# Kernel optimization log

Hardware: AMD Instinct MI355X
Metric: run time of the kernel (lower is better)

## Reference

```python
import jax, jax.numpy as jnp
import numpy as np

INV_148 = 1.0 / 1.48  # scaling to align grids with flat-top gaussian


def _trilinear_sample(grid, pts):
    # grid: [C, D, H, W]; pts: [N, 3] in (x,y,z)=(W,H,D) normalized coords, align_corners=True,
    # padding_mode='zeros' (out-of-bounds corners contribute 0). Returns [C, N].
    C, D, H, W = grid.shape
    fx = (pts[:, 0] + 1.0) * 0.5 * (W - 1)
    fy = (pts[:, 1] + 1.0) * 0.5 * (H - 1)
    fz = (pts[:, 2] + 1.0) * 0.5 * (D - 1)
    x0 = jnp.floor(fx).astype(jnp.int32)
    y0 = jnp.floor(fy).astype(jnp.int32)
    z0 = jnp.floor(fz).astype(jnp.int32)
    wx, wy, wz = fx - x0, fy - y0, fz - z0
    out = jnp.zeros((C, pts.shape[0]), dtype=grid.dtype)
    for dz in (0, 1):
        for dy in (0, 1):
            for dx in (0, 1):
                xi, yi, zi = x0 + dx, y0 + dy, z0 + dz
                w = (wx if dx else 1.0 - wx) * (wy if dy else 1.0 - wy) * (wz if dz else 1.0 - wz)
                valid = ((xi >= 0) & (xi < W) & (yi >= 0) & (yi < H) & (zi >= 0) & (zi < D))
                v = grid[:, jnp.clip(zi, 0, D - 1), jnp.clip(yi, 0, H - 1), jnp.clip(xi, 0, W - 1)]
                out = out + v * (w * valid)
    return out


def setup_inputs() -> dict:
    key = jax.random.key(0)
    ks = jax.random.split(key, 10)
    G, Fch, Dg, N, NPL, OUT = 32, 2, 64, 524288, 64, 1
    in_dim = G * Fch
    x = jax.random.uniform(ks[0], (N, 3), minval=-1.0, maxval=1.0, dtype=jnp.float32)
    grid_scales = jax.random.uniform(ks[1], (G, 3), minval=1.5, maxval=2.5, dtype=jnp.float32)
    grid_translations = jax.random.uniform(ks[2], (G, 3), minval=-1.0, maxval=1.0, dtype=jnp.float32) * (grid_scales - 1.0)
    feature_grids = jax.random.uniform(ks[3], (G, Fch, Dg, Dg, Dg), minval=-0.001, maxval=0.001, dtype=jnp.float32)
    W0 = jax.random.normal(ks[4], (NPL, in_dim), dtype=jnp.float32) * (1.0 / np.sqrt(in_dim))
    b0 = jnp.zeros((NPL,), dtype=jnp.float32)
    W1 = jax.random.normal(ks[5], (NPL, NPL), dtype=jnp.float32) * (1.0 / np.sqrt(NPL))
    b1 = jnp.zeros((NPL,), dtype=jnp.float32)
    W2 = jax.random.normal(ks[6], (OUT, NPL), dtype=jnp.float32) * (1.0 / np.sqrt(NPL))
    b2 = jnp.zeros((OUT,), dtype=jnp.float32)
    return {"x": x, "grid_scales": grid_scales, "grid_translations": grid_translations,
            "feature_grids": feature_grids, "W0": W0, "b0": b0, "W1": W1, "b1": b1, "W2": W2, "b2": b2}


def reference(x, grid_scales, grid_translations, feature_grids, W0, b0, W1, b1, W2, b2):
    G = feature_grids.shape[0]
    N = x.shape[0]
    # transform(): per-grid affine (diag scale + translation), then * 1/1.48 -> [G, N, 3]
    local = (x[None, :, :] * grid_scales[:, None, :] + grid_translations[:, None, :]) * INV_148
    # forward detaches grid coords before grid_sample
    local = jax.lax.stop_gradient(local)
    feats = jax.vmap(_trilinear_sample)(feature_grids, local)  # [G, F, N]
    h = feats.reshape(G * feats.shape[1], N).T  # [N, G*F]
    h = jax.nn.relu(h @ W0.T + b0)
    h = jax.nn.relu(h @ W1.T + b1)
    return h @ W2.T + b2  # [N, n_outputs]
```

## Files before the change

### kernel.cpp

```cpp
#include <hip/hip_runtime.h>
#include <hip/hip_fp16.h>

#define NG    32
#define DG    64
#define NPL   64
#define CPD   8
#define NCELL 512
#define HPAD  16
#define BS    512
#define NPT   3
#define TV    4096

typedef _Float16 half8 __attribute__((ext_vector_type(8)));
typedef float    floatx4 __attribute__((ext_vector_type(4)));

__global__ void pack_grids_kernel(const float* __restrict__ fg,
                                  uint4* __restrict__ pg, int total4) {
    int idx = blockIdx.x * blockDim.x + threadIdx.x;
    if (idx >= total4) return;
    int g  = idx >> 16;
    int v4 = (idx & 65535) << 2;
    const float* base = fg + ((size_t)g << 19);
    float4 a = *(const float4*)(base + v4);
    float4 b = *(const float4*)(base + (1 << 18) + v4);
    uint4 o;
    __half2 h;
    h = __floats2half2_rn(a.x, b.x); o.x = *(unsigned*)&h;
    h = __floats2half2_rn(a.y, b.y); o.y = *(unsigned*)&h;
    h = __floats2half2_rn(a.z, b.z); o.z = *(unsigned*)&h;
    h = __floats2half2_rn(a.w, b.w); o.w = *(unsigned*)&h;
    pg[idx] = o;
}

__device__ __forceinline__ int morton8(int cx, int cy, int cz) {
    return  (cx & 1)              | ((cy & 1) << 1)        | ((cz & 1) << 2)
         | (((cx >> 1) & 1) << 3) | (((cy >> 1) & 1) << 4) | (((cz >> 1) & 1) << 5)
         | (((cx >> 2) & 1) << 6) | (((cy >> 2) & 1) << 7) | (((cz >> 2) & 1) << 8);
}
__device__ __forceinline__ int cell_of(float px, float py, float pz) {
    int cx = min(max((int)((px + 1.0f) * (0.5f * CPD)), 0), CPD - 1);
    int cy = min(max((int)((py + 1.0f) * (0.5f * CPD)), 0), CPD - 1);
    int cz = min(max((int)((pz + 1.0f) * (0.5f * CPD)), 0), CPD - 1);
    return morton8(cx, cy, cz);
}

__global__ __launch_bounds__(BS)
void hist_kernel(const float* __restrict__ x, int N, int* __restrict__ ghist) {
    __shared__ int lh[NCELL];
    for (int i = threadIdx.x; i < NCELL; i += BS) lh[i] = 0;
    __syncthreads();
    int n = blockIdx.x * BS + threadIdx.x;
    if (n < N) atomicAdd(&lh[cell_of(x[3*n], x[3*n+1], x[3*n+2])], 1);
    __syncthreads();
    for (int i = threadIdx.x; i < NCELL; i += BS) {
        int c = lh[i];
        if (c) atomicAdd(&ghist[i * HPAD], c);
    }
}

__global__ __launch_bounds__(NCELL)
void scan_kernel(const int* __restrict__ ghist, int* __restrict__ gcursor,
                 int* __restrict__ cellstart) {
    __shared__ int buf[NCELL];
    int t = threadIdx.x;
    int v = ghist[t * HPAD];
    buf[t] = v;
    __syncthreads();
    #pragma unroll
    for (int off = 1; off < NCELL; off <<= 1) {
        int u = (t >= off) ? buf[t - off] : 0;
        __syncthreads();
        buf[t] += u;
        __syncthreads();
    }
    int excl = buf[t] - v;
    gcursor[t * HPAD] = excl;
    cellstart[t] = excl;
    if (t == NCELL - 1) cellstart[NCELL] = buf[t];
}

__global__ __launch_bounds__(BS)
void scatter_kernel(const float* __restrict__ x, int N,
                    int* __restrict__ gcursor, float4* __restrict__ sorted,
                    int* __restrict__ nidx) {
    __shared__ int cnt[NCELL];
    __shared__ int base[NCELL];
    int tid = threadIdx.x;
    for (int i = tid; i < NCELL; i += BS) cnt[i] = 0;
    __syncthreads();
    int n = blockIdx.x * BS + tid;
    float px = 0.f, py = 0.f, pz = 0.f;
    int c = 0, r = 0;
    bool act = (n < N);
    if (act) {
        px = x[3*n]; py = x[3*n+1]; pz = x[3*n+2];
        c = cell_of(px, py, pz);
        r = atomicAdd(&cnt[c], 1);
    }
    __syncthreads();
    for (int i = tid; i < NCELL; i += BS) {
        int cc = cnt[i];
        base[i] = cc ? atomicAdd(&gcursor[i * HPAD], cc) : 0;
    }
    __syncthreads();
    if (act) {
        int pos = base[c] + r;
        sorted[pos] = make_float4(px, py, pz, 0.0f);
        nidx[pos]   = n;
    }
}

__device__ __forceinline__ float2 h2_to_f2(unsigned u) {
    __half2 h = *reinterpret_cast<__half2*>(&u);
    return __half22float2(h);
}

__global__ __launch_bounds__(BS)
void gather_kernel(const float4* __restrict__ sorted,
                   const int*   __restrict__ cellstart,
                   const float* __restrict__ scales,
                   const float* __restrict__ trans,
                   const unsigned* __restrict__ pg,
                   int4* __restrict__ featbuf, int N)
{
    __shared__ float    sA[NG * 3];
    __shared__ float    sB[NG * 3];
    __shared__ int      sO[NG * 3];
    __shared__ unsigned tile[2][TV];

    const int tid = threadIdx.x;
    int bid = blockIdx.x;
    int c   = ((bid & 7) << 6) + (bid >> 3);

    int s0 = cellstart[c];
    int e  = cellstart[c + 1];

    int cx = (c & 1)        | (((c >> 3) & 1) << 1) | (((c >> 6) & 1) << 2);
    int cy = ((c >> 1) & 1) | (((c >> 4) & 1) << 1) | (((c >> 7) & 1) << 2);
    int cz = ((c >> 2) & 1) | (((c >> 5) & 1) << 1) | (((c >> 8) & 1) << 2);

    if (tid < NG * 3) {
        const float k = (1.0f / 1.48f) * 31.5f;
        float A  = scales[tid] * k;
        float Bv = trans[tid] * k + 31.5f;
        sA[tid] = A; sB[tid] = Bv;
        int d  = tid % 3;
        int cc = (d == 0) ? cx : ((d == 1) ? cy : cz);
        int o  = (int)floorf(fmaf((float)cc * 0.25f - 1.0f, A, Bv));
        sO[tid] = min(max(o, 0), 48);
    }

    float px[NPT], py[NPT], pz[NPT];
    int   ip[NPT];
    bool  act[NPT];
    #pragma unroll
    for (int p = 0; p < NPT; ++p) {
        int i = s0 + (p << 9) + tid;
        ip[p]  = i;
        act[p] = (i < e);
        if (act[p]) {
            float4 q = sorted[i];
            px[p] = q.x; py[p] = q.y; pz[p] = q.z;
        } else { px[p] = py[p] = pz[p] = 0.f; }
    }
    __syncthreads();

    {
        int ox = sO[0], oy = sO[1], oz = sO[2];
        #pragma unroll
        for (int j = 0; j < 8; ++j) {
            int v = tid + (j << 9);
            tile[0][v] = pg[((oz + (v >> 8)) << 12) + ((oy + ((v >> 4) & 15)) << 6)
                            + ox + (v & 15)];
        }
    }
    __syncthreads();

    unsigned fp[NPT][4];
    unsigned r[8];

    #pragma unroll
    for (int g = 0; g < NG; ++g) {
        const int cur = g & 1;

        if (g < NG - 1) {
            int ox = sO[3*g+3], oy = sO[3*g+4], oz = sO[3*g+5];
            const unsigned* gb = pg + ((size_t)(g + 1) << 18);
            #pragma unroll
            for (int j = 0; j < 8; ++j) {
                int v = tid + (j << 9);
                r[j] = gb[((oz + (v >> 8)) << 12) + ((oy + ((v >> 4) & 15)) << 6)
                          + ox + (v & 15)];
            }
        }

        {
            const unsigned* tl = tile[cur];
            float A0 = sA[3*g+0], A1 = sA[3*g+1], A2 = sA[3*g+2];
            float B0 = sB[3*g+0], B1 = sB[3*g+1], B2 = sB[3*g+2];
            int ox = sO[3*g+0], oy = sO[3*g+1], oz = sO[3*g+2];
            #pragma unroll
            for (int p = 0; p < NPT; ++p) {
                if (!act[p]) { fp[p][g & 3] = 0; continue; }
                float fx = fmaf(px[p], A0, B0);
                float fy = fmaf(py[p], A1, B1);
                float fz = fmaf(pz[p], A2, B2);
                float flx = floorf(fx), fly = floorf(fy), flz = floorf(fz);
                int x0 = (int)flx, y0 = (int)fly, z0 = (int)flz;
                float wx = fx - flx, wy = fy - fly, wz = fz - flz;

                float wxa0 = (x0 >= 0  && x0     < DG) ? (1.0f - wx) : 0.0f;
                float wxa1 = (x0 >= -1 && x0 + 1 < DG) ? wx          : 0.0f;
                float wya0 = (y0 >= 0  && y0     < DG) ? (1.0f - wy) : 0.0f;
                float wya1 = (y0 >= -1 && y0 + 1 < DG) ? wy          : 0.0f;
                float wza0 = (z0 >= 0  && z0     < DG) ? (1.0f - wz) : 0.0f;
                float wza1 = (z0 >= -1 && z0 + 1 < DG) ? wz          : 0.0f;

                int ix0 = min(max(x0     - ox, 0), 15);
                int ix1 = min(max(x0 + 1 - ox, 0), 15);
                int iy0 = (min(max(y0     - oy, 0), 15)) << 4;
                int iy1 = (min(max(y0 + 1 - oy, 0), 15)) << 4;
                int iz0 = (min(max(z0     - oz, 0), 15)) << 8;
                int iz1 = (min(max(z0 + 1 - oz, 0), 15)) << 8;

                float w00 = wya0 * wza0, w10 = wya1 * wza0;
                float w01 = wya0 * wza1, w11 = wya1 * wza1;

                float c0 = 0.0f, c1 = 0.0f;
                float2 v;
                v = h2_to_f2(tl[iz0 + iy0 + ix0]); c0 = fmaf(wxa0*w00, v.x, c0); c1 = fmaf(wxa0*w00, v.y, c1);
                v = h2_to_f2(tl[iz0 + iy0 + ix1]); c0 = fmaf(wxa1*w00, v.x, c0); c1 = fmaf(wxa1*w00, v.y, c1);
                v = h2_to_f2(tl[iz0 + iy1 + ix0]); c0 = fmaf(wxa0*w10, v.x, c0); c1 = fmaf(wxa0*w10, v.y, c1);
                v = h2_to_f2(tl[iz0 + iy1 + ix1]); c0 = fmaf(wxa1*w10, v.x, c0); c1 = fmaf(wxa1*w10, v.y, c1);
                v = h2_to_f2(tl[iz1 + iy0 + ix0]); c0 = fmaf(wxa0*w01, v.x, c0); c1 = fmaf(wxa0*w01, v.y, c1);
                v = h2_to_f2(tl[iz1 + iy0 + ix1]); c0 = fmaf(wxa1*w01, v.x, c0); c1 = fmaf(wxa1*w01, v.y, c1);
                v = h2_to_f2(tl[iz1 + iy1 + ix0]); c0 = fmaf(wxa0*w11, v.x, c0); c1 = fmaf(wxa0*w11, v.y, c1);
                v = h2_to_f2(tl[iz1 + iy1 + ix1]); c0 = fmaf(wxa1*w11, v.x, c0); c1 = fmaf(wxa1*w11, v.y, c1);

                __half2 hv = __floats2half2_rn(c0, c1);
                fp[p][g & 3] = *reinterpret_cast<unsigned*>(&hv);
            }
        }

        if (g < NG - 1) {
            #pragma unroll
            for (int j = 0; j < 8; ++j) tile[cur ^ 1][tid + (j << 9)] = r[j];
        }

        if ((g & 3) == 3) {
            const size_t plane = (size_t)(g >> 2) * (size_t)N;
            #pragma unroll
            for (int p = 0; p < NPT; ++p)
                if (act[p])
                    featbuf[plane + ip[p]] =
                        make_int4((int)fp[p][0], (int)fp[p][1],
                                  (int)fp[p][2], (int)fp[p][3]);
        }

        __syncthreads();
    }
}

#define MBS 256
__global__ __launch_bounds__(MBS)
void mlp_kernel(const int4* __restrict__ featbuf,
                const int* __restrict__ nidx,
                const float* __restrict__ W0, const float* __restrict__ b0,
                const float* __restrict__ W1, const float* __restrict__ b1,
                const float* __restrict__ W2, const float* __restrict__ b2,
                float* __restrict__ out, int N)
{
    __shared__ _Float16 sW0h[NPL * NPL];
    __shared__ _Float16 sW1h[NPL * NPL];
    __shared__ float    sb0f[NPL], sb1f[NPL], sW2f[NPL];
    __shared__ _Float16 sH[4][NPL * NPL];

    int tid = threadIdx.x;
    for (int i = tid; i < NPL * NPL; i += MBS) {
        sW0h[i] = (_Float16)W0[i];
        sW1h[i] = (_Float16)W1[i];
    }
    if (tid < NPL) { sb0f[tid] = b0[tid]; sb1f[tid] = b1[tid]; sW2f[tid] = W2[tid]; }
    __syncthreads();

    const int wave = tid >> 6;
    const int lane = tid & 63;
    const int l15  = lane & 15;
    const int kg   = lane >> 4;
    const long wbase = (long)blockIdx.x * MBS + wave * 64;
    if (wbase >= N) return;

    half8 B0[4][2], B1[4][2];
    float bias0[4], bias1[4], w2v[4];
    #pragma unroll
    for (int nt = 0; nt < 4; ++nt) {
        int ch = nt * 16 + l15;
        #pragma unroll
        for (int kh = 0; kh < 2; ++kh) {
            int k = kh * 32 + kg * 8;
            B0[nt][kh] = *(const half8*)&sW0h[ch * NPL + k];
            B1[nt][kh] = *(const half8*)&sW1h[ch * NPL + k];
        }
        bias0[nt] = sb0f[ch];
        bias1[nt] = sb1f[ch];
        w2v[nt]   = sW2f[ch];
    }

    _Float16* H = &sH[wave][0];

    floatx4 acc[4][4];
    #pragma unroll
    for (int mt = 0; mt < 4; ++mt) {
        long pt = wbase + mt * 16 + l15;
        if (pt > N - 1) pt = N - 1;
        int4 t0 = featbuf[(size_t)kg * N + pt];
        int4 t1 = featbuf[(size_t)(4 + kg) * N + pt];
        half8 a0 = *reinterpret_cast<half8*>(&t0);
        half8 a1 = *reinterpret_cast<half8*>(&t1);
        #pragma unroll
        for (int nt = 0; nt < 4; ++nt) {
            floatx4 cc = {0.f, 0.f, 0.f, 0.f};
            cc = __builtin_amdgcn_mfma_f32_16x16x32_f16(a0, B0[nt][0], cc, 0, 0, 0);
            cc = __builtin_amdgcn_mfma_f32_16x16x32_f16(a1, B0[nt][1], cc, 0, 0, 0);
            acc[mt][nt] = cc;
        }
    }
    #pragma unroll
    for (int mt = 0; mt < 4; ++mt)
        #pragma unroll
        for (int nt = 0; nt < 4; ++nt) {
            int ch = nt * 16 + l15;
            #pragma unroll
            for (int r = 0; r < 4; ++r) {
                float v = fmaxf(acc[mt][nt][r] + bias0[nt], 0.0f);
                H[(mt * 16 + kg * 4 + r) * NPL + ch] = (_Float16)v;
            }
        }

    floatx4 acc2[4][4];
    #pragma unroll
    for (int mt = 0; mt < 4; ++mt) {
        const _Float16* hp = &H[(mt * 16 + l15) * NPL];
        half8 a0 = *(const half8*)&hp[kg * 8];
        half8 a1 = *(const half8*)&hp[32 + kg * 8];
        #pragma unroll
        for (int nt = 0; nt < 4; ++nt) {
            floatx4 cc = {0.f, 0.f, 0.f, 0.f};
            cc = __builtin_amdgcn_mfma_f32_16x16x32_f16(a0, B1[nt][0], cc, 0, 0, 0);
            cc = __builtin_amdgcn_mfma_f32_16x16x32_f16(a1, B1[nt][1], cc, 0, 0, 0);
            acc2[mt][nt] = cc;
        }
    }

    float p[4][4];
    #pragma unroll
    for (int mt = 0; mt < 4; ++mt)
        #pragma unroll
        for (int r = 0; r < 4; ++r) p[mt][r] = 0.0f;
    #pragma unroll
    for (int mt = 0; mt < 4; ++mt)
        #pragma unroll
        for (int nt = 0; nt < 4; ++nt)
            #pragma unroll
            for (int r = 0; r < 4; ++r) {
                float v = fmaxf(acc2[mt][nt][r] + bias1[nt], 0.0f);
                p[mt][r] = fmaf(v, w2v[nt], p[mt][r]);
            }
    #pragma unroll
    for (int mt = 0; mt < 4; ++mt)
        #pragma unroll
        for (int r = 0; r < 4; ++r) {
            float s = p[mt][r];
            s += __shfl_xor(s, 1);
            s += __shfl_xor(s, 2);
            s += __shfl_xor(s, 4);
            s += __shfl_xor(s, 8);
            p[mt][r] = s;
        }

    float* HF = (float*)H;
    float ob = b2[0];
    if (l15 == 0) {
        #pragma unroll
        for (int mt = 0; mt < 4; ++mt)
            #pragma unroll
            for (int r = 0; r < 4; ++r)
                HF[mt * 16 + kg * 4 + r] = p[mt][r] + ob;
    }
    long pos = wbase + lane;
    if (pos < N) out[nidx[pos]] = HF[lane];
}

__global__ __launch_bounds__(256)
void fused_fallback_kernel(const float* __restrict__ x,
                           const float* __restrict__ scales,
                           const float* __restrict__ trans,
                           const __half2* __restrict__ pg,
                           const float* __restrict__ W0, const float* __restrict__ b0,
                           const float* __restrict__ W1, const float* __restrict__ b1,
                           const float* __restrict__ W2, const float* __restrict__ b2,
                           float* __restrict__ out, int N)
{
    __shared__ float sW0[NPL*NPL], sW1[NPL*NPL], sW2[NPL], sb0[NPL], sb1[NPL];
    __shared__ float sA[NG*3], sB[NG*3];
    const int tid = threadIdx.x;
    for (int i = tid; i < NPL*NPL; i += 256) { sW0[i] = W0[i]; sW1[i] = W1[i]; }
    if (tid < NPL) { sW2[tid] = W2[tid]; sb0[tid] = b0[tid]; sb1[tid] = b1[tid]; }
    if (tid < NG*3) {
        const float k = (1.0f / 1.48f) * 31.5f;
        sA[tid] = scales[tid] * k;
        sB[tid] = trans[tid] * k + 31.5f;
    }
    __syncthreads();
    int n = blockIdx.x * 256 + tid;
    if (n >= N) return;
    float px = x[3*n], py = x[3*n+1], pz = x[3*n+2];
    float feat[2*NG];
    #pragma unroll
    for (int g = 0; g < NG; ++g) {
        float fx = fmaf(px, sA[3*g+0], sB[3*g+0]);
        float fy = fmaf(py, sA[3*g+1], sB[3*g+1]);
        float fz = fmaf(pz, sA[3*g+2], sB[3*g+2]);
        float c0 = 0.f, c1 = 0.f;
        if (fx > -1.f && fx < 64.f && fy > -1.f && fy < 64.f && fz > -1.f && fz < 64.f) {
            float flx = floorf(fx), fly = floorf(fy), flz = floorf(fz);
            int x0 = (int)flx, y0 = (int)fly, z0 = (int)flz;
            float wx = fx-flx, wy = fy-fly, wz = fz-flz;
            float wxa[2], wya[2], wza[2]; int xia[2], yia[2], zia[2];
            wxa[0] = (x0 >= 0  && x0   < DG) ? (1.f-wx) : 0.f;
            wxa[1] = (x0 >= -1 && x0+1 < DG) ? wx : 0.f;
            wya[0] = (y0 >= 0  && y0   < DG) ? (1.f-wy) : 0.f;
            wya[1] = (y0 >= -1 && y0+1 < DG) ? wy : 0.f;
            wza[0] = (z0 >= 0  && z0   < DG) ? (1.f-wz) : 0.f;
            wza[1] = (z0 >= -1 && z0+1 < DG) ? wz : 0.f;
            xia[0] = min(max(x0,0),DG-1); xia[1] = min(max(x0+1,0),DG-1);
            yia[0] = min(max(y0,0),DG-1); yia[1] = min(max(y0+1,0),DG-1);
            zia[0] = min(max(z0,0),DG-1); zia[1] = min(max(z0+1,0),DG-1);
            #pragma unroll
            for (int dz = 0; dz < 2; ++dz)
                #pragma unroll
                for (int dy = 0; dy < 2; ++dy) {
                    int rowoff = (zia[dz] << 12) + (yia[dy] << 6);
                    float wyz = wya[dy] * wza[dz];
                    #pragma unroll
                    for (int dx = 0; dx < 2; ++dx) {
                        float w = wxa[dx] * wyz;
                        float2 vf = __half22float2(pg[(g << 18) + rowoff + xia[dx]]);
                        c0 = fmaf(w, vf.x, c0); c1 = fmaf(w, vf.y, c1);
                    }
                }
        }
        feat[2*g] = c0; feat[2*g+1] = c1;
    }
    float h1[NPL];
    #pragma unroll
    for (int j = 0; j < NPL; j += 2) {
        float a0=0.f,a1=0.f,a2=0.f,a3=0.f;
        const float* r0 = &sW0[j*NPL]; const float* r1 = &sW0[(j+1)*NPL];
        #pragma unroll
        for (int k = 0; k < NPL; k += 2) {
            a0 = fmaf(feat[k],r0[k],a0); a1 = fmaf(feat[k+1],r0[k+1],a1);
            a2 = fmaf(feat[k],r1[k],a2); a3 = fmaf(feat[k+1],r1[k+1],a3);
        }
        h1[j] = fmaxf((a0+a1)+sb0[j],0.f); h1[j+1] = fmaxf((a2+a3)+sb0[j+1],0.f);
    }
    #pragma unroll
    for (int j = 0; j < NPL; j += 2) {
        float a0=0.f,a1=0.f,a2=0.f,a3=0.f;
        const float* r0 = &sW1[j*NPL]; const float* r1 = &sW1[(j+1)*NPL];
        #pragma unroll
        for (int k = 0; k < NPL; k += 2) {
            a0 = fmaf(h1[k],r0[k],a0); a1 = fmaf(h1[k+1],r0[k+1],a1);
            a2 = fmaf(h1[k],r1[k],a2); a3 = fmaf(h1[k+1],r1[k+1],a3);
        }
        feat[j] = fmaxf((a0+a1)+sb1[j],0.f); feat[j+1] = fmaxf((a2+a3)+sb1[j+1],0.f);
    }
    float a0 = 0.f, a1 = 0.f;
    #pragma unroll
    for (int k = 0; k < NPL; k += 2) { a0 = fmaf(feat[k],sW2[k],a0); a1 = fmaf(feat[k+1],sW2[k+1],a1); }
    out[n] = (a0+a1) + b2[0];
}

extern "C" void kernel_launch(void* const* d_in, const int* in_sizes, int n_in,
                              void* d_out, int out_size, void* d_ws, size_t ws_size,
                              hipStream_t stream) {
    const float* x  = (const float*)d_in[0];
    const float* gs = (const float*)d_in[1];
    const float* gt = (const float*)d_in[2];
    const float* fg = (const float*)d_in[3];
    const float* W0 = (const float*)d_in[4];
    const float* b0 = (const float*)d_in[5];
    const float* W1 = (const float*)d_in[6];
    const float* b1 = (const float*)d_in[7];
    const float* W2 = (const float*)d_in[8];
    const float* b2 = (const float*)d_in[9];
    float* out = (float*)d_out;

    const int N = out_size;

    const size_t pg_bytes   = (size_t)NG * (1 << 18) * 4;
    const size_t feat_bytes = (size_t)N * 8 * sizeof(int4);
    const size_t sort_bytes = (size_t)N * sizeof(float4);
    const size_t nidx_bytes = (size_t)N * sizeof(int);
    const size_t cs_bytes   = ((NCELL + 1 + 15) & ~15) * sizeof(int);
    const size_t hist_bytes = (size_t)NCELL * HPAD * sizeof(int);
    const size_t need_full  = pg_bytes + feat_bytes + sort_bytes + nidx_bytes
                            + cs_bytes + 2 * hist_bytes;

    if (ws_size >= need_full) {
        char* w = (char*)d_ws;
        unsigned* pg        = (unsigned*)w;  w += pg_bytes;
        int4*     featbuf   = (int4*)w;      w += feat_bytes;
        float4*   sorted    = (float4*)w;    w += sort_bytes;
        int*      nidx      = (int*)w;       w += nidx_bytes;
        int*      cellstart = (int*)w;       w += cs_bytes;
        int*      ghist     = (int*)w;       w += hist_bytes;
        int*      gcur      = (int*)w;

        int total4 = NG << 16;
        int nblk   = (N + BS - 1) / BS;
        pack_grids_kernel<<<(total4 + 255) / 256, 256, 0, stream>>>(fg, (uint4*)pg, total4);
        hipMemsetAsync(ghist, 0, hist_bytes, stream);
        hist_kernel<<<nblk, BS, 0, stream>>>(x, N, ghist);
        scan_kernel<<<1, NCELL, 0, stream>>>(ghist, gcur, cellstart);
        scatter_kernel<<<nblk, BS, 0, stream>>>(x, N, gcur, sorted, nidx);
        gather_kernel<<<NCELL, BS, 0, stream>>>(
            sorted, cellstart, gs, gt, pg, featbuf, N);
        mlp_kernel<<<(N + MBS - 1) / MBS, MBS, 0, stream>>>(
            featbuf, nidx, W0, b0, W1, b1, W2, b2, out, N);
    } else if (ws_size >= pg_bytes) {
        unsigned* pg = (unsigned*)d_ws;
        int total4 = NG << 16;
        pack_grids_kernel<<<(total4 + 255) / 256, 256, 0, stream>>>(fg, (uint4*)pg, total4);
        fused_fallback_kernel<<<(N + 255) / 256, 256, 0, stream>>>(
            x, gs, gt, (const __half2*)pg, W0, b0, W1, b1, W2, b2, out, N);
    } else {
        fused_fallback_kernel<<<(N + 255) / 256, 256, 0, stream>>>(
            x, gs, gt, (const __half2*)fg, W0, b0, W1, b1, W2, b2, out, N);
    }
}
```

Baseline: 185.7 us.

## Sort into finer cells, split gather blocks, skip out-of-range grids per cell

After: 189.3 us. No clear change (+2.0%).

```diff
diff --git a/kernel.cpp b/kernel.cpp
--- a/kernel.cpp
+++ b/kernel.cpp
@@ -4,12 +4,13 @@
 #define NG    32
 #define DG    64
 #define NPL   64
-#define CPD   8
+#define CPD2  16
+#define NC2   4096
 #define NCELL 512
-#define HPAD  16
+#define HPAD  4
 #define BS    512
-#define NPT   3
 #define TV    4096
+#define HS    68
 
 typedef _Float16 half8 __attribute__((ext_vector_type(8)));
 typedef float    floatx4 __attribute__((ext_vector_type(4)));
@@ -32,61 +33,70 @@
     pg[idx] = o;
 }
 
-__device__ __forceinline__ int morton8(int cx, int cy, int cz) {
-    return  (cx & 1)              | ((cy & 1) << 1)        | ((cz & 1) << 2)
-         | (((cx >> 1) & 1) << 3) | (((cy >> 1) & 1) << 4) | (((cz >> 1) & 1) << 5)
-         | (((cx >> 2) & 1) << 6) | (((cy >> 2) & 1) << 7) | (((cz >> 2) & 1) << 8);
+__device__ __forceinline__ int morton16(int cx, int cy, int cz) {
+    int m = 0;
+    #pragma unroll
+    for (int b = 0; b < 4; ++b)
+        m |= (((cx >> b) & 1) << (3 * b))
+           | (((cy >> b) & 1) << (3 * b + 1))
+           | (((cz >> b) & 1) << (3 * b + 2));
+    return m;
 }
 __device__ __forceinline__ int cell_of(float px, float py, float pz) {
-    int cx = min(max((int)((px + 1.0f) * (0.5f * CPD)), 0), CPD - 1);
-    int cy = min(max((int)((py + 1.0f) * (0.5f * CPD)), 0), CPD - 1);
-    int cz = min(max((int)((pz + 1.0f) * (0.5f * CPD)), 0), CPD - 1);
-    return morton8(cx, cy, cz);
+    int cx = min(max((int)((px + 1.0f) * (0.5f * CPD2)), 0), CPD2 - 1);
+    int cy = min(max((int)((py + 1.0f) * (0.5f * CPD2)), 0), CPD2 - 1);
+    int cz = min(max((int)((pz + 1.0f) * (0.5f * CPD2)), 0), CPD2 - 1);
+    return morton16(cx, cy, cz);
 }
 
 __global__ __launch_bounds__(BS)
 void hist_kernel(const float* __restrict__ x, int N, int* __restrict__ ghist) {
-    __shared__ int lh[NCELL];
-    for (int i = threadIdx.x; i < NCELL; i += BS) lh[i] = 0;
+    __shared__ int lh[NC2];
+    for (int i = threadIdx.x; i < NC2; i += BS) lh[i] = 0;
     __syncthreads();
     int n = blockIdx.x * BS + threadIdx.x;
     if (n < N) atomicAdd(&lh[cell_of(x[3*n], x[3*n+1], x[3*n+2])], 1);
     __syncthreads();
-    for (int i = threadIdx.x; i < NCELL; i += BS) {
+    for (int i = threadIdx.x; i < NC2; i += BS) {
         int c = lh[i];
         if (c) atomicAdd(&ghist[i * HPAD], c);
     }
 }
 
-__global__ __launch_bounds__(NCELL)
+__global__ __launch_bounds__(1024)
 void scan_kernel(const int* __restrict__ ghist, int* __restrict__ gcursor,
                  int* __restrict__ cellstart) {
-    __shared__ int buf[NCELL];
+    __shared__ int tsum[1024];
     int t = threadIdx.x;
-    int v = ghist[t * HPAD];
-    buf[t] = v;
-    __syncthreads();
-    #pragma unroll
-    for (int off = 1; off < NCELL; off <<= 1) {
-        int u = (t >= off) ? buf[t - off] : 0;
+    int v0 = ghist[(t * 4 + 0) * HPAD];
+    int v1 = ghist[(t * 4 + 1) * HPAD];
+    int v2 = ghist[(t * 4 + 2) * HPAD];
+    int v3 = ghist[(t * 4 + 3) * HPAD];
+    tsum[t] = v0 + v1 + v2 + v3;
+    __syncthreads();
+    #pragma unroll
+    for (int off = 1; off < 1024; off <<= 1) {
+        int u = (t >= off) ? tsum[t - off] : 0;
         __syncthreads();
-        buf[t] += u;
+        tsum[t] += u;
         __syncthreads();
     }
-    int excl = buf[t] - v;
-    gcursor[t * HPAD] = excl;
-    cellstart[t] = excl;
-    if (t == NCELL - 1) cellstart[NCELL] = buf[t];
+    int base = (t == 0) ? 0 : tsum[t - 1];
+    gcursor[(t*4+0)*HPAD] = base; cellstart[t*4+0] = base; base += v0;
+    gcursor[(t*4+1)*HPAD] = base; cellstart[t*4+1] = base; base += v1;
+    gcursor[(t*4+2)*HPAD] = base; cellstart[t*4+2] = base; base += v2;
+    gcursor[(t*4+3)*HPAD] = base; cellstart[t*4+3] = base;
+    if (t == 1023) cellstart[NC2] = tsum[1023];
 }
 
 __global__ __launch_bounds__(BS)
 void scatter_kernel(const float* __restrict__ x, int N,
                     int* __restrict__ gcursor, float4* __restrict__ sorted,
                     int* __restrict__ nidx) {
-    __shared__ int cnt[NCELL];
-    __shared__ int base[NCELL];
+    __shared__ int cnt[NC2];
+    __shared__ int base[NC2];
     int tid = threadIdx.x;
-    for (int i = tid; i < NCELL; i += BS) cnt[i] = 0;
+    for (int i = tid; i < NC2; i += BS) cnt[i] = 0;
     __syncthreads();
     int n = blockIdx.x * BS + tid;
     float px = 0.f, py = 0.f, pz = 0.f;
@@ -98,7 +108,7 @@
         r = atomicAdd(&cnt[c], 1);
     }
     __syncthreads();
-    for (int i = tid; i < NCELL; i += BS) {
+    for (int i = tid; i < NC2; i += BS) {
         int cc = cnt[i];
         base[i] = cc ? atomicAdd(&gcursor[i * HPAD], cc) : 0;
     }
@@ -115,9 +125,61 @@
     return __half22float2(h);
 }
 
+template<bool FAST>
+__device__ __forceinline__ unsigned sample_tile(
+    const unsigned* __restrict__ tl,
+    float px, float py, float pz,
+    float A0, float A1, float A2, float B0, float B1, float B2,
+    int ox, int oy, int oz)
+{
+    float fx = fmaf(px, A0, B0);
+    float fy = fmaf(py, A1, B1);
+    float fz = fmaf(pz, A2, B2);
+    float flx = floorf(fx), fly = floorf(fy), flz = floorf(fz);
+    int x0 = (int)flx, y0 = (int)fly, z0 = (int)flz;
+    float wx = fx - flx, wy = fy - fly, wz = fz - flz;
+
+    float wxa0, wxa1, wya0, wya1, wza0, wza1;
+    if (FAST) {
+        wxa0 = 1.0f - wx; wxa1 = wx;
+        wya0 = 1.0f - wy; wya1 = wy;
+        wza0 = 1.0f - wz; wza1 = wz;
+    } else {
+        wxa0 = (x0 >= 0  && x0     < DG) ? (1.0f - wx) : 0.0f;
+        wxa1 = (x0 >= -1 && x0 + 1 < DG) ? wx          : 0.0f;
+        wya0 = (y0 >= 0  && y0     < DG) ? (1.0f - wy) : 0.0f;
+        wya1 = (y0 >= -1 && y0 + 1 < DG) ? wy          : 0.0f;
+        wza0 = (z0 >= 0  && z0     < DG) ? (1.0f - wz) : 0.0f;
+        wza1 = (z0 >= -1 && z0 + 1 < DG) ? wz          : 0.0f;
+    }
+    int ix0 = min(max(x0     - ox, 0), 15);
+    int ix1 = min(max(x0 + 1 - ox, 0), 15);
+    int iy0 = (min(max(y0     - oy, 0), 15)) << 4;
+    int iy1 = (min(max(y0 + 1 - oy, 0), 15)) << 4;
+    int iz0 = (min(max(z0     - oz, 0), 15)) << 8;
+    int iz1 = (min(max(z0 + 1 - oz, 0), 15)) << 8;
+
+    float w00 = wya0 * wza0, w10 = wya1 * wza0;
+    float w01 = wya0 * wza1, w11 = wya1 * wza1;
+
+    float c0 = 0.0f, c1 = 0.0f;
+    float2 v;
+    v = h2_to_f2(tl[iz0+iy0+ix0]); c0 = fmaf(wxa0*w00, v.x, c0); c1 = fmaf(wxa0*w00, v.y, c1);
+    v = h2_to_f2(tl[iz0+iy0+ix1]); c0 = fmaf(wxa1*w00, v.x, c0); c1 = fmaf(wxa1*w00, v.y, c1);
+    v = h2_to_f2(tl[iz0+iy1+ix0]); c0 = fmaf(wxa0*w10, v.x, c0); c1 = fmaf(wxa0*w10, v.y, c1);
+    v = h2_to_f2(tl[iz0+iy1+ix1]); c0 = fmaf(wxa1*w10, v.x, c0); c1 = fmaf(wxa1*w10, v.y, c1);
+    v = h2_to_f2(tl[iz1+iy0+ix0]); c0 = fmaf(wxa0*w01, v.x, c0); c1 = fmaf(wxa0*w01, v.y, c1);
+    v = h2_to_f2(tl[iz1+iy0+ix1]); c0 = fmaf(wxa1*w01, v.x, c0); c1 = fmaf(wxa1*w01, v.y, c1);
+    v = h2_to_f2(tl[iz1+iy1+ix0]); c0 = fmaf(wxa0*w11, v.x, c0); c1 = fmaf(wxa0*w11, v.y, c1);
+    v = h2_to_f2(tl[iz1+iy1+ix1]); c0 = fmaf(wxa1*w11, v.x, c0); c1 = fmaf(wxa1*w11, v.y, c1);
+
+    __half2 hv = __floats2half2_rn(c0, c1);
+    return *reinterpret_cast<unsigned*>(&hv);
+}
+
 __global__ __launch_bounds__(BS)
 void gather_kernel(const float4* __restrict__ sorted,
-                   const int*   __restrict__ cellstart,
+                   const int*   __restrict__ cs16,
                    const float* __restrict__ scales,
                    const float* __restrict__ trans,
                    const unsigned* __restrict__ pg,
@@ -126,14 +188,23 @@
     __shared__ float    sA[NG * 3];
     __shared__ float    sB[NG * 3];
     __shared__ int      sO[NG * 3];
+    __shared__ int      sCls[NG];
+    __shared__ int      sList[NG + 1];
     __shared__ unsigned tile[2][TV];
 
-    const int tid = threadIdx.x;
-    int bid = blockIdx.x;
-    int c   = ((bid & 7) << 6) + (bid >> 3);
-
-    int s0 = cellstart[c];
-    int e  = cellstart[c + 1];
+    const int tid  = threadIdx.x;
+    const int bid  = blockIdx.x;
+    const int half = bid >> 9;
+    const int cell = bid & 511;
+    const int c    = ((cell & 7) << 6) + (cell >> 3);
+
+    int s0c = cs16[c * 8];
+    int ec  = cs16[c * 8 + 8];
+    int cnt = ec - s0c;
+    int hsz = (cnt + 1) >> 1;
+    int start = s0c + half * hsz;
+    int end   = min(ec, start + hsz);
+    if (start >= end) return;
 
     int cx = (c & 1)        | (((c >> 3) & 1) << 1) | (((c >> 6) & 1) << 2);
     int cy = ((c >> 1) & 1) | (((c >> 4) & 1) << 1) | (((c >> 7) & 1) << 2);
@@ -149,115 +220,102 @@
         int o  = (int)floorf(fmaf((float)cc * 0.25f - 1.0f, A, Bv));
         sO[tid] = min(max(o, 0), 48);
     }
-
-    float px[NPT], py[NPT], pz[NPT];
-    int   ip[NPT];
-    bool  act[NPT];
-    #pragma unroll
-    for (int p = 0; p < NPT; ++p) {
-        int i = s0 + (p << 9) + tid;
-        ip[p]  = i;
-        act[p] = (i < e);
-        if (act[p]) {
-            float4 q = sorted[i];
-            px[p] = q.x; py[p] = q.y; pz[p] = q.z;
-        } else { px[p] = py[p] = pz[p] = 0.f; }
-    }
-    __syncthreads();
-
-    {
-        int ox = sO[0], oy = sO[1], oz = sO[2];
-        #pragma unroll
-        for (int j = 0; j < 8; ++j) {
-            int v = tid + (j << 9);
-            tile[0][v] = pg[((oz + (v >> 8)) << 12) + ((oy + ((v >> 4) & 15)) << 6)
+    __syncthreads();
+    if (tid < NG) {
+        bool skip = false, fast = true;
+        #pragma unroll
+        for (int d = 0; d < 3; ++d) {
+            float A = sA[3 * tid + d], B = sB[3 * tid + d];
+            int  cc = (d == 0) ? cx : ((d == 1) ? cy : cz);
+            float lo = fmaf((float)cc, 0.25f, -1.0f) - 1e-4f;
+            float hi = lo + 0.25f + 2e-4f;
+            float fmn = fmaf(lo, A, B);
+            float fmx = fmaf(hi, A, B);
+            skip = skip || (fmx <= -1.0f) || (fmn >= 64.0f);
+            fast = fast && (fmn >= 0.0f) && (fmx <= 63.0f);
+        }
+        sCls[tid] = skip ? 0 : (fast ? 1 : 2);
+    }
+    __syncthreads();
+    if (tid == 0) {
+        int n2 = 0;
+        for (int g = 0; g < NG; ++g)
+            if (sCls[g]) sList[n2++] = g;
+        sList[NG] = n2;
+    }
+    __syncthreads();
+    const int nAct = sList[NG];
+
+    int  ip0 = start + tid,        ip1 = start + BS + tid;
+    bool act0 = (ip0 < end),       act1 = (ip1 < end);
+    float px0 = 0.f, py0 = 0.f, pz0 = 0.f;
+    float px1 = 0.f, py1 = 0.f, pz1 = 0.f;
+    if (act0) { float4 q = sorted[ip0]; px0 = q.x; py0 = q.y; pz0 = q.z; }
+    if (act1) { float4 q = sorted[ip1]; px1 = q.x; py1 = q.y; pz1 = q.z; }
+
+    if (nAct > 0) {
+        int g0 = sList[0];
+        int ox = sO[3*g0], oy = sO[3*g0+1], oz = sO[3*g0+2];
+        const unsigned* gb = pg + ((size_t)g0 << 18);
+        #pragma unroll
+        for (int jj = 0; jj < 8; ++jj) {
+            int v = tid + (jj << 9);
+            tile[0][v] = gb[((oz + (v >> 8)) << 12) + ((oy + ((v >> 4) & 15)) << 6)
                             + ox + (v & 15)];
         }
     }
     __syncthreads();
 
-    unsigned fp[NPT][4];
+    unsigned fp0[4], fp1[4];
     unsigned r[8];
-
-    #pragma unroll
-    for (int g = 0; g < NG; ++g) {
-        const int cur = g & 1;
-
-        if (g < NG - 1) {
-            int ox = sO[3*g+3], oy = sO[3*g+4], oz = sO[3*g+5];
-            const unsigned* gb = pg + ((size_t)(g + 1) << 18);
-            #pragma unroll
-            for (int j = 0; j < 8; ++j) {
-                int v = tid + (j << 9);
-                r[j] = gb[((oz + (v >> 8)) << 12) + ((oy + ((v >> 4) & 15)) << 6)
-                          + ox + (v & 15)];
+    int j = 0;
+
+    #pragma unroll 1
+    for (int w = 0; w < 8; ++w) {
+        #pragma unroll
+        for (int q = 0; q < 4; ++q) {
+            int g   = 4 * w + q;
+            int cls = sCls[g];
+            if (cls == 0) { fp0[q] = 0u; fp1[q] = 0u; continue; }
+
+            const unsigned* tl = &tile[j & 1][0];
+            bool more = (j + 1 < nAct);
+            if (more) {
+                int gn = sList[j + 1];
+                int ox = sO[3*gn], oy = sO[3*gn+1], oz = sO[3*gn+2];
+                const unsigned* gb = pg + ((size_t)gn << 18);
+                #pragma unroll
+                for (int jj = 0; jj < 8; ++jj) {
+                    int v = tid + (jj << 9);
+                    r[jj] = gb[((oz + (v >> 8)) << 12) + ((oy + ((v >> 4) & 15)) << 6)
+                               + ox + (v & 15)];
+                }
             }
-        }
-
-        {
-            const unsigned* tl = tile[cur];
-            float A0 = sA[3*g+0], A1 = sA[3*g+1], A2 = sA[3*g+2];
-            float B0 = sB[3*g+0], B1 = sB[3*g+1], B2 = sB[3*g+2];
-            int ox = sO[3*g+0], oy = sO[3*g+1], oz = sO[3*g+2];
-            #pragma unroll
-            for (int p = 0; p < NPT; ++p) {
-                if (!act[p]) { fp[p][g & 3] = 0; continue; }
-                float fx = fmaf(px[p], A0, B0);
-                float fy = fmaf(py[p], A1, B1);
-                float fz = fmaf(pz[p], A2, B2);
-                float flx = floorf(fx), fly = floorf(fy), flz = floorf(fz);
-                int x0 = (int)flx, y0 = (int)fly, z0 = (int)flz;
-                float wx = fx - flx, wy = fy - fly, wz = fz - flz;
-
-                float wxa0 = (x0 >= 0  && x0     < DG) ? (1.0f - wx) : 0.0f;
-                float wxa1 = (x0 >= -1 && x0 + 1 < DG) ? wx          : 0.0f;
-                float wya0 = (y0 >= 0  && y0     < DG) ? (1.0f - wy) : 0.0f;
-                float wya1 = (y0 >= -1 && y0 + 1 < DG) ? wy          : 0.0f;
-                float wza0 = (z0 >= 0  && z0     < DG) ? (1.0f - wz) : 0.0f;
-                float wza1 = (z0 >= -1 && z0 + 1 < DG) ? wz          : 0.0f;
-
-                int ix0 = min(max(x0     - ox, 0), 15);
-                int ix1 = min(max(x0 + 1 - ox, 0), 15);
-                int iy0 = (min(max(y0     - oy, 0), 15)) << 4;
-                int iy1 = (min(max(y0 + 1 - oy, 0), 15)) << 4;
-                int iz0 = (min(max(z0     - oz, 0), 15)) << 8;
-                int iz1 = (min(max(z0 + 1 - oz, 0), 15)) << 8;
-
-                float w00 = wya0 * wza0, w10 = wya1 * wza0;
-                float w01 = wya0 * wza1, w11 = wya1 * wza1;
-
-                float c0 = 0.0f, c1 = 0.0f;
-                float2 v;
-                v = h2_to_f2(tl[iz0 + iy0 + ix0]); c0 = fmaf(wxa0*w00, v.x, c0); c1 = fmaf(wxa0*w00, v.y, c1);
-                v = h2_to_f2(tl[iz0 + iy0 + ix1]); c0 = fmaf(wxa1*w00, v.x, c0); c1 = fmaf(wxa1*w00, v.y, c1);
-                v = h2_to_f2(tl[iz0 + iy1 + ix0]); c0 = fmaf(wxa0*w10, v.x, c0); c1 = fmaf(wxa0*w10, v.y, c1);
-                v = h2_to_f2(tl[iz0 + iy1 + ix1]); c0 = fmaf(wxa1*w10, v.x, c0); c1 = fmaf(wxa1*w10, v.y, c1);
-                v = h2_to_f2(tl[iz1 + iy0 + ix0]); c0 = fmaf(wxa0*w01, v.x, c0); c1 = fmaf(wxa0*w01, v.y, c1);
-                v = h2_to_f2(tl[iz1 + iy0 + ix1]); c0 = fmaf(wxa1*w01, v.x, c0); c1 = fmaf(wxa1*w01, v.y, c1);
-                v = h2_to_f2(tl[iz1 + iy1 + ix0]); c0 = fmaf(wxa0*w11, v.x, c0); c1 = fmaf(wxa0*w11, v.y, c1);
-                v = h2_to_f2(tl[iz1 + iy1 + ix1]); c0 = fmaf(wxa1*w11, v.x, c0); c1 = fmaf(wxa1*w11, v.y, c1);
-
-                __half2 hv = __floats2half2_rn(c0, c1);
-                fp[p][g & 3] = *reinterpret_cast<unsigned*>(&hv);
+
+            float A0 = sA[3*g], A1 = sA[3*g+1], A2 = sA[3*g+2];
+            float B0 = sB[3*g], B1 = sB[3*g+1], B2 = sB[3*g+2];
+            int   ox = sO[3*g], oy = sO[3*g+1], oz = sO[3*g+2];
+            if (cls == 1) {
+                fp0[q] = act0 ? sample_tile<true >(tl, px0,py0,pz0, A0,A1,A2,B0,B1,B2, ox,oy,oz) : 0u;
+                fp1[q] = act1 ? sample_tile<true >(tl, px1,py1,pz1, A0,A1,A2,B0,B1,B2, ox,oy,oz) : 0u;
+            } else {
+                fp0[q] = act0 ? sample_tile<false>(tl, px0,py0,pz0, A0,A1,A2,B0,B1,B2, ox,oy,oz) : 0u;
+                fp1[q] = act1 ? sample_tile<false>(tl, px1,py1,pz1, A0,A1,A2,B0,B1,B2, ox,oy,oz) : 0u;
             }
-        }
-
-        if (g < NG - 1) {
-            #pragma unroll
-            for (int j = 0; j < 8; ++j) tile[cur ^ 1][tid + (j << 9)] = r[j];
-        }
-
-        if ((g & 3) == 3) {
-            const size_t plane = (size_t)(g >> 2) * (size_t)N;
-            #pragma unroll
-            for (int p = 0; p < NPT; ++p)
-                if (act[p])
-                    featbuf[plane + ip[p]] =
-                        make_int4((int)fp[p][0], (int)fp[p][1],
-                                  (int)fp[p][2], (int)fp[p][3]);
-        }
-
-        __syncthreads();
+
+            if (more) {
+                unsigned* td = &tile[(j & 1) ^ 1][0];
+                #pragma unroll
+                for (int jj = 0; jj < 8; ++jj) td[tid + (jj << 9)] = r[jj];
+            }
+            __syncthreads();
+            ++j;
+        }
+        const size_t plane = (size_t)w * (size_t)N;
+        if (act0) featbuf[plane + ip0] =
+            make_int4((int)fp0[0], (int)fp0[1], (int)fp0[2], (int)fp0[3]);
+        if (act1) featbuf[plane + ip1] =
+            make_int4((int)fp1[0], (int)fp1[1], (int)fp1[2], (int)fp1[3]);
     }
 }
 
@@ -270,10 +328,10 @@
                 const float* __restrict__ W2, const float* __restrict__ b2,
                 float* __restrict__ out, int N)
 {
-    __shared__ _Float16 sW0h[NPL * NPL];
-    __shared__ _Float16 sW1h[NPL * NPL];
-    __shared__ float    sb0f[NPL], sb1f[NPL], sW2f[NPL];
-    __shared__ _Float16 sH[4][NPL * NPL];
+    __shared__ __align__(16) _Float16 sW0h[NPL * NPL];
+    __shared__ __align__(16) _Float16 sW1h[NPL * NPL];
+    __shared__ float sb0f[NPL], sb1f[NPL], sW2f[NPL];
+    __shared__ __align__(16) _Float16 sH[4][NPL * HS];
 
     int tid = threadIdx.x;
     for (int i = tid; i < NPL * NPL; i += MBS) {
@@ -333,14 +391,14 @@
             #pragma unroll
             for (int r = 0; r < 4; ++r) {
                 float v = fmaxf(acc[mt][nt][r] + bias0[nt], 0.0f);
-                H[(mt * 16 + kg * 4 + r) * NPL + ch] = (_Float16)v;
+                H[(mt * 16 + kg * 4 + r) * HS + ch] = (_Float16)v;
             }
         }
 
     floatx4 acc2[4][4];
     #pragma unroll
     for (int mt = 0; mt < 4; ++mt) {
-        const _Float16* hp = &H[(mt * 16 + l15) * NPL];
+        const _Float16* hp = &H[(mt * 16 + l15) * HS];
         half8 a0 = *(const half8*)&hp[kg * 8];
         half8 a1 = *(const half8*)&hp[32 + kg * 8];
         #pragma unroll
@@ -502,8 +560,8 @@
     const size_t feat_bytes = (size_t)N * 8 * sizeof(int4);
     const size_t sort_bytes = (size_t)N * sizeof(float4);
     const size_t nidx_bytes = (size_t)N * sizeof(int);
-    const size_t cs_bytes   = ((NCELL + 1 + 15) & ~15) * sizeof(int);
-    const size_t hist_bytes = (size_t)NCELL * HPAD * sizeof(int);
+    const size_t cs_bytes   = ((NC2 + 1 + 15) & ~15) * sizeof(int);
+    const size_t hist_bytes = (size_t)NC2 * HPAD * sizeof(int);
     const size_t need_full  = pg_bytes + feat_bytes + sort_bytes + nidx_bytes
                             + cs_bytes + 2 * hist_bytes;
 
@@ -522,9 +580,9 @@
         pack_grids_kernel<<<(total4 + 255) / 256, 256, 0, stream>>>(fg, (uint4*)pg, total4);
         hipMemsetAsync(ghist, 0, hist_bytes, stream);
         hist_kernel<<<nblk, BS, 0, stream>>>(x, N, ghist);
-        scan_kernel<<<1, NCELL, 0, stream>>>(ghist, gcur, cellstart);
+        scan_kernel<<<1, 1024, 0, stream>>>(ghist, gcur, cellstart);
         scatter_kernel<<<nblk, BS, 0, stream>>>(x, N, gcur, sorted, nidx);
-        gather_kernel<<<NCELL, BS, 0, stream>>>(
+        gather_kernel<<<NCELL * 2, BS, 0, stream>>>(
             sorted, cellstart, gs, gt, pg, featbuf, N);
         mlp_kernel<<<(N + MBS - 1) / MBS, MBS, 0, stream>>>(
             featbuf, nidx, W0, b0, W1, b1, W2, b2, out, N);
```
